# Optimization experiments

Hardware: AMD Instinct MI355X
Metric: run time of the kernel (lower is better)

The kernel has to match this reference:

```python
import jax, jax.numpy as jnp
import numpy as np


def _build_ring_index(H):
    """Precompute static (row, col) source-index maps for the square
    rotational unrolling. Output maps have shape [ceil(H/2), 4*H].

    For ring i (from center outward, dif = lmid - i), each output row is the
    concatenation of 9 segments exactly matching the torch slice/repeat/flip
    sequence, totalling 4H-4 columns, then the first 4 columns are copied to
    the last 4 (the tail wrap in the original code).
    """
    W = H
    lmid = (H - 1) // 2
    Hr = (H + 1) // 2
    rows = np.zeros((Hr, 4 * H), dtype=np.int32)
    cols = np.zeros((Hr, 4 * H), dtype=np.int32)
    for i in range(lmid, -1, -1):
        dif = lmid - i
        el = 2 * dif if H % 2 == 1 else 2 * dif + 1
        r, c = [], []
        # corner (i,i) repeated i times
        r += [i] * i;                    c += [i] * i
        # top edge, left-to-right
        r += [i] * el;                   c += list(range(i, i + el))
        # top-right corner repeated 2i
        r += [i] * (2 * i);              c += [W - i - 1] * (2 * i)
        # right edge, top-to-bottom
        r += list(range(i, i + el));     c += [W - i - 1] * el
        # bottom-right corner repeated 2i
        r += [i + el] * (2 * i);         c += [i + el] * (2 * i)
        # bottom edge, right-to-left (fliplr of img[i+el, i+1:i+1+el])
        r += [i + el] * el;              c += list(range(i + el, i, -1))
        # bottom-left corner repeated 2i
        r += [i + el] * (2 * i);         c += [i] * (2 * i)
        # left edge, bottom-to-top (fliplr of img[i+1:i+1+el, i])
        r += list(range(i + el, i, -1)); c += [i] * el
        # corner (i,i) repeated i times
        r += [i] * i;                    c += [i] * i
        # total length is always 4H-4; wrap first 4 entries to the tail
        r += r[:4];                      c += c[:4]
        rows[dif] = r
        cols[dif] = c
    return rows, cols


def setup_inputs() -> dict:
    key = jax.random.key(0)
    x = jax.random.normal(key, (16, 32, 512, 512), dtype=jnp.float32)
    return {"x": x}


def reference(x) -> jnp.ndarray:
    B, C, H, W = x.shape
    rows, cols = _build_ring_index(H)  # static, shape [ceil(H/2), 4H]
    # single fused gather replacing the ring-wise python loop
    return x[:, :, jnp.asarray(rows), jnp.asarray(cols)]
```

## Files before the change

kernel.cpp:

```cpp
#include <hip/hip_runtime.h>


#define SQRL_H 512
#define SQRL_IMG ((size_t)SQRL_H * SQRL_H)
#define SQRL_ROWW 2048
#define NB_PER_IMG 72

__global__ __launch_bounds__(256) void sqrl_kernel(
    const float* __restrict__ x, float* __restrict__ outf, long n4, long nB) {
    __shared__ float lds[64][65];
    const long bid = blockIdx.x;

    if (bid < nB) {
        const int  rem  = (int)(bid % NB_PER_IMG);
        const long img  = bid / NB_PER_IMG;
        const int  jt   = rem % 9;
        const int  dt   = (rem / 9) & 3;
        const int  side = rem / 36;
        const int  dif0 = dt * 64;
        const int  j0   = (side == 0 ? 448 : 1472) + 64 * jt;
        const int  ctr  = (side == 0) ? 766 : 1788;

        int jmin;
        if (j0 <= ctr && ctr < j0 + 64) jmin = 0;
        else {
            int a = j0 - ctr;        if (a < 0) a = -a;
            int b = j0 + 63 - ctr;   if (b < 0) b = -b;
            jmin = a < b ? a : b;
        }
        const int dmax = dif0 + 63;
        if (dmax < jmin) return;

        const int rlo = (side == 0) ? (j0 - 511) : (1981 - j0);
        const int clo = (side == 0) ? (256 + dif0) : (192 - dif0);
        const int rc  = (side == 0) ? 255 : 256;
        const float* __restrict__ base = x + img * SQRL_IMG;
        const int t = (int)threadIdx.x;

        {
            const int lr = t >> 2;
            const int q  = t & 3;
            const int r  = rlo + lr;
            if ((unsigned)r < 512u) {
                int adr = r - rc; if (adr < 0) adr = -adr;
                if (adr <= dmax) {
                    const float* rowp = base + (size_t)r * SQRL_H;
#pragma unroll
                    for (int k = 0; k < 4; ++k) {
                        const int c0 = (q + 4 * k) * 4;
                        const bool need = (side == 0)
                            ? (clo + c0 + 3 >= 256 + adr)
                            : (clo + c0     <= 255 - adr);
                        if (need) {
                            const float4 v = *reinterpret_cast<const float4*>(rowp + clo + c0);
                            lds[lr][c0 + 0] = v.x;
                            lds[lr][c0 + 1] = v.y;
                            lds[lr][c0 + 2] = v.z;
                            lds[lr][c0 + 3] = v.w;
                        }
                    }
                }
            }
        }
        __syncthreads();

        const int jl   = t & 63;
        const int dgrp = t >> 6;
        const int j    = j0 + jl;
        int adj = j - ctr; if (adj < 0) adj = -adj;
        const int lj = (side == 0) ? jl : (63 - jl);
        float* const orow = outf + ((size_t)img * 256 + dif0) * SQRL_ROWW + j;
#pragma unroll
        for (int it = 0; it < 16; ++it) {
            const int dl = dgrp + 4 * it;
            if (dif0 + dl >= adj) {
                const int lc = (side == 0) ? dl : (63 - dl);
                orow[(size_t)dl * SQRL_ROWW] = lds[lj][lc];
            }
        }
        return;
    }

    const long tA = (bid - nB) * 256 + threadIdx.x;
    if (tA >= n4) return;

    const int  j4  = (int)(tA & 511);
    const long row = tA >> 9;
    const int  dif = (int)(row & 255);
    const long img = row >> 8;
    const float* __restrict__ base = x + img * SQRL_IMG;

    const int i_ = 255 - dif;
    const int el = 2 * dif + 1;
    const int b1 = i_ + el;
    const int b2 = b1 + 2 * i_;
    const int b3 = b2 + el;
    const int b4 = b3 + 2 * i_;
    const int b5 = b4 + el;
    const int b6 = b5 + 2 * i_;
    const int b7 = b6 + el;

    const int j0 = j4 * 4;
    float4 v;
    float* vp = reinterpret_cast<float*>(&v);
    unsigned vm = 0;
#pragma unroll
    for (int k = 0; k < 4; ++k) {
        const int j  = j0 + k;
        const int jj = (j >= 2044) ? (j - 2044) : j;
        const bool vert = (jj >= b2 && jj < b3) || (jj >= b6 && jj < b7);
        if (vert) { vm |= 1u << k; vp[k] = 0.0f; continue; }
        int r, c;
        if (jj < b1)      { r = i_;       c = (jj > i_) ? jj : i_; }
        else if (jj < b3) { c = 511 - i_; int d = jj - b2; r = i_ + (d > 0 ? d : 0); }
        else if (jj < b5) { r = b1;       int d = jj - b4; c = b1 - (d > 0 ? d : 0); }
        else if (jj < b7) { c = i_;       int d = jj - b6; r = b1 - (d > 0 ? d : 0); }
        else              { r = i_;       c = i_; }
        vp[k] = base[(size_t)r * SQRL_H + c];
    }
    if (vm == 0u) {
        *reinterpret_cast<float4*>(outf + (size_t)tA * 4) = v;
    } else if (vm != 15u) {
#pragma unroll
        for (int k = 0; k < 4; ++k)
            if (!(vm & (1u << k))) outf[(size_t)tA * 4 + k] = vp[k];
    }
}

extern "C" void kernel_launch(void* const* d_in, const int* in_sizes, int n_in,
                              void* d_out, int out_size, void* d_ws, size_t ws_size,
                              hipStream_t stream) {
    const float* x = (const float*)d_in[0];
    float* outf = (float*)d_out;
    long n4   = (long)out_size / 4;
    long nA   = (n4 + 255) / 256;
    long nimg = n4 >> 17;
    long nB   = nimg * NB_PER_IMG;
    long nblocks = nA + nB;
    sqrl_kernel<<<dim3((unsigned)nblocks), dim3(256), 0, stream>>>(x, outf, n4, nB);
}
```

Measured before the change: 1.714 ms.

## Process one output row per block with segment-classified vector loads and nontemporal stores

The horizontal-edge path now assigns one output ring row per block, with each thread handling two float4 chunks. The four corner values are loaded once per row and broadcast. Chunks lying entirely inside a segment are written with a single vector load (or a reversed pair of float2 loads) instead of four scalar gathers. Output writes use nontemporal stores to avoid polluting the cache, at the cost of more branching per chunk.

```diff
diff --git a/kernel.cpp b/kernel.cpp
--- a/kernel.cpp
+++ b/kernel.cpp
@@ -6,8 +6,10 @@
 #define SQRL_ROWW 2048
 #define NB_PER_IMG 72
 
+typedef float f32x4 __attribute__((ext_vector_type(4)));
+
 __global__ __launch_bounds__(256) void sqrl_kernel(
-    const float* __restrict__ x, float* __restrict__ outf, long n4, long nB) {
+    const float* __restrict__ x, float* __restrict__ outf, long nB) {
     __shared__ float lds[64][65];
     const long bid = blockIdx.x;
 
@@ -52,7 +54,7 @@
                             ? (clo + c0 + 3 >= 256 + adr)
                             : (clo + c0     <= 255 - adr);
                         if (need) {
-                            const float4 v = *reinterpret_cast<const float4*>(rowp + clo + c0);
+                            const f32x4 v = *reinterpret_cast<const f32x4*>(rowp + clo + c0);
                             lds[lr][c0 + 0] = v.x;
                             lds[lr][c0 + 1] = v.y;
                             lds[lr][c0 + 2] = v.z;
@@ -81,49 +83,87 @@
         return;
     }
 
-    const long tA = (bid - nB) * 256 + threadIdx.x;
-    if (tA >= n4) return;
-
-    const int  j4  = (int)(tA & 511);
-    const long row = tA >> 9;
-    const int  dif = (int)(row & 255);
-    const long img = row >> 8;
+    const long rowid = bid - nB;
+    const int  dif = (int)(rowid & 255);
+    const long img = rowid >> 8;
     const float* __restrict__ base = x + img * SQRL_IMG;
+    float* __restrict__ orow = outf + (size_t)rowid * SQRL_ROWW;
 
     const int i_ = 255 - dif;
-    const int el = 2 * dif + 1;
-    const int b1 = i_ + el;
-    const int b2 = b1 + 2 * i_;
-    const int b3 = b2 + el;
-    const int b4 = b3 + 2 * i_;
-    const int b5 = b4 + el;
-    const int b6 = b5 + 2 * i_;
-    const int b7 = b6 + el;
+    const int b1 = 256 + dif;
+    const int b2 = 766 - dif,  b3 = 767 + dif;
+    const int b4 = 1277 - dif, b5 = 1278 + dif;
+    const int b6 = 1788 - dif, b7 = 1789 + dif;
 
-    const int j0 = j4 * 4;
-    float4 v;
-    float* vp = reinterpret_cast<float*>(&v);
-    unsigned vm = 0;
+    const float c_tl = base[i_ * 512 + i_];
+    const float c_tr = base[i_ * 512 + b1];
+    const float c_br = base[b1 * 512 + b1];
+    const float c_bl = base[b1 * 512 + i_];
+    const float* __restrict__ toprow = base + i_ * 512;
+    const float* __restrict__ botrow = base + b1 * 512;
+
+    const int t = (int)threadIdx.x;
 #pragma unroll
-    for (int k = 0; k < 4; ++k) {
-        const int j  = j0 + k;
-        const int jj = (j >= 2044) ? (j - 2044) : j;
-        const bool vert = (jj >= b2 && jj < b3) || (jj >= b6 && jj < b7);
-        if (vert) { vm |= 1u << k; vp[k] = 0.0f; continue; }
-        int r, c;
-        if (jj < b1)      { r = i_;       c = (jj > i_) ? jj : i_; }
-        else if (jj < b3) { c = 511 - i_; int d = jj - b2; r = i_ + (d > 0 ? d : 0); }
-        else if (jj < b5) { r = b1;       int d = jj - b4; c = b1 - (d > 0 ? d : 0); }
-        else if (jj < b7) { c = i_;       int d = jj - b6; r = b1 - (d > 0 ? d : 0); }
-        else              { r = i_;       c = i_; }
-        vp[k] = base[(size_t)r * SQRL_H + c];
-    }
-    if (vm == 0u) {
-        *reinterpret_cast<float4*>(outf + (size_t)tA * 4) = v;
-    } else if (vm != 15u) {
+    for (int h = 0; h < 2; ++h) {
+        const int p0 = (t + 256 * h) * 4;
+
+        auto seg = [&](int p) -> int {
+            if (p < i_)   return 0;
+            if (p < b1)   return 1;
+            if (p < b2)   return 2;
+            if (p < b3)   return 3;
+            if (p < b4)   return 4;
+            if (p < b5)   return 5;
+            if (p < b6)   return 6;
+            if (p < b7)   return 7;
+            if (p < 2044) return 8;
+            return 9;
+        };
+        const int sA = seg(p0), sB = seg(p0 + 3);
+
+        if (sA == sB && sA != 9) {
+            if (sA == 3 || sA == 7) continue;
+            f32x4 v;
+            if (sA == 1) {
+                v = *reinterpret_cast<const f32x4*>(toprow + p0);
+            } else if (sA == 5) {
+                const int a0 = b1 - (p0 - b4);
+                const float2 lo = *reinterpret_cast<const float2*>(botrow + a0 - 3);
+                const float2 hi = *reinterpret_cast<const float2*>(botrow + a0 - 1);
+                v.x = hi.y; v.y = hi.x; v.z = lo.y; v.w = lo.x;
+            } else {
+                const float cv = (sA == 2) ? c_tr : (sA == 4) ? c_br
+                               : (sA == 6) ? c_bl : c_tl;
+                v.x = cv; v.y = cv; v.z = cv; v.w = cv;
+            }
+            __builtin_nontemporal_store(v, reinterpret_cast<f32x4*>(orow + p0));
+        } else {
+            float vals[4]; unsigned vm = 0;
 #pragma unroll
-        for (int k = 0; k < 4; ++k)
-            if (!(vm & (1u << k))) outf[(size_t)tA * 4 + k] = vp[k];
+            for (int k = 0; k < 4; ++k) {
+                const int p = p0 + k;
+                float val;
+                if (p < i_)        val = c_tl;
+                else if (p < b1)   val = toprow[p];
+                else if (p < b2)   val = c_tr;
+                else if (p < b3)   { vm |= 1u << k; val = 0.0f; }
+                else if (p < b4)   val = c_br;
+                else if (p < b5)   val = botrow[b1 - (p - b4)];
+                else if (p < b6)   val = c_bl;
+                else if (p < b7)   { vm |= 1u << k; val = 0.0f; }
+                else if (p < 2044) val = c_tl;
+                else { const int p2 = p - 2044; val = (p2 < i_) ? c_tl : toprow[p2]; }
+                vals[k] = val;
+            }
+            if (vm == 0u) {
+                f32x4 v; v.x = vals[0]; v.y = vals[1]; v.z = vals[2]; v.w = vals[3];
+                __builtin_nontemporal_store(v, reinterpret_cast<f32x4*>(orow + p0));
+            } else if (vm != 15u) {
+#pragma unroll
+                for (int k = 0; k < 4; ++k)
+                    if (!(vm & (1u << k))) orow[p0 + k] = vals[k];
+            }
+        }
     }
 }
 
@@ -133,9 +173,9 @@
     const float* x = (const float*)d_in[0];
     float* outf = (float*)d_out;
     long n4   = (long)out_size / 4;
-    long nA   = (n4 + 255) / 256;
     long nimg = n4 >> 17;
     long nB   = nimg * NB_PER_IMG;
-    long nblocks = nA + nB;
-    sqrl_kernel<<<dim3((unsigned)nblocks), dim3(256), 0, stream>>>(x, outf, n4, nB);
+    long nA   = nimg * 256;
+    long nblocks = nB + nA;
+    sqrl_kernel<<<dim3((unsigned)nblocks), dim3(256), 0, stream>>>(x, outf, nB);
 }
```

Result: faster. 1.608 ms (-6.2%).
